# Kernel tuning notes

Hardware: AMD Instinct MI355X
Metric: run time of the kernel (lower is better)

The kernel has to match this reference:

```python
import jax, jax.numpy as jnp
import numpy as np

N_NODES = 50000
N_EDGES = 800000
IN_FEAT = 128
OUT_FEAT = 128


def _glorot(key, shape):
    fan_in, fan_out = shape[1], shape[0]
    lim = jnp.sqrt(6.0 / (fan_in + fan_out))
    return jax.random.uniform(key, shape, jnp.float32, -lim, lim)


def setup_inputs() -> dict:
    key = jax.random.key(0)
    ks = jax.random.split(key, 9)
    x = jax.random.normal(ks[0], (N_NODES, IN_FEAT), jnp.float32)
    edge_index = jax.random.randint(ks[1], (2, N_EDGES), 0, N_NODES, jnp.int64)
    # SAGEConv params: lin_l applied to aggregated neighbors (with bias),
    # lin_r applied to root features (no bias) -- PyG default mean aggregation.
    W1l = _glorot(ks[2], (OUT_FEAT, IN_FEAT)); b1l = jnp.zeros((OUT_FEAT,), jnp.float32)
    W1r = _glorot(ks[3], (OUT_FEAT, IN_FEAT))
    W2l = _glorot(ks[4], (OUT_FEAT, OUT_FEAT)); b2l = jnp.zeros((OUT_FEAT,), jnp.float32)
    W2r = _glorot(ks[5], (OUT_FEAT, OUT_FEAT))
    Wlin = _glorot(ks[6], (2, OUT_FEAT)); blin = jnp.zeros((2,), jnp.float32)
    return {"x": x, "edge_index": edge_index,
            "W1l": W1l, "b1l": b1l, "W1r": W1r,
            "W2l": W2l, "b2l": b2l, "W2r": W2r,
            "Wlin": Wlin, "blin": blin}


def _sage_conv(x, src, dst, Wl, bl, Wr, n_nodes):
    # mean-aggregate neighbor features at destination nodes
    agg_sum = jax.ops.segment_sum(x[src], dst, num_segments=n_nodes)  # [N, F]
    deg = jax.ops.segment_sum(jnp.ones((src.shape[0],), x.dtype), dst, num_segments=n_nodes)
    agg = agg_sum / jnp.maximum(deg, 1.0)[:, None]
    return agg @ Wl.T + bl + x @ Wr.T


def reference(x, edge_index, W1l, b1l, W1r, W2l, b2l, W2r, Wlin, blin):
    src, dst = edge_index[0], edge_index[1]
    n = x.shape[0]
    h = _sage_conv(x, src, dst, W1l, b1l, W1r, n)
    h = jax.nn.relu(h)  # dropout is identity in eval mode
    h = _sage_conv(h, src, dst, W2l, b2l, W2r, n)
    h = jax.nn.relu(h)
    logits = h @ Wlin.T + blin  # [N, 2]
    return jax.nn.log_softmax(logits, axis=1)
```

## Files before the change

kernel.cpp:

```cpp
#include <hip/hip_runtime.h>
#include <math.h>

#define N_NODES 50000
#define N_EDGES 800000
#define F 128
#define ELL_CAP 64
#define NSHARD 8
#define RANKS 128
#define EPR (N_EDGES / RANKS)
#define NPS (N_NODES / NSHARD)
#define EDGE_BLKS (NSHARD * RANKS)
#define CVT_BLKS 6250

typedef __attribute__((ext_vector_type(8))) short short8;
typedef __attribute__((ext_vector_type(4))) float float4v;

__device__ inline unsigned short f2bf(float f) {
    unsigned int u = __builtin_bit_cast(unsigned int, f);
    u += 0x7FFF + ((u >> 16) & 1);
    return (unsigned short)(u >> 16);
}
__device__ inline float bf2f_lo(unsigned int u) {
    return __builtin_bit_cast(float, u << 16);
}
__device__ inline float bf2f_hi(unsigned int u) {
    return __builtin_bit_cast(float, u & 0xFFFF0000u);
}

__global__ __launch_bounds__(256) void prep(const float* __restrict__ x,
                                            const int* __restrict__ src,
                                            const int* __restrict__ dst,
                                            const float* __restrict__ W1l,
                                            const float* __restrict__ W1r,
                                            const float* __restrict__ W2l,
                                            const float* __restrict__ W2r,
                                            unsigned short* __restrict__ xb,
                                            int* __restrict__ cnt,
                                            unsigned short* __restrict__ nbr,
                                            unsigned short* __restrict__ P1,
                                            unsigned short* __restrict__ P2) {
    int blk = blockIdx.x;
    if (blk < EDGE_BLKS) {
        int shard = blk & 7;
        int rank = blk >> 3;
        int lo = shard * NPS, hi = lo + NPS;
        int base = rank * EPR;
        for (int i = threadIdx.x; i < EPR; i += 256) {
            int d = dst[base + i];
            if (d >= lo && d < hi) {
                int s = src[base + i];
                int pos = atomicAdd(&cnt[d], 1);
                if (pos < ELL_CAP)
                    nbr[d * ELL_CAP + pos] = (unsigned short)s;
            }
        }
    } else if (blk < EDGE_BLKS + CVT_BLKS) {
        int i = (blk - EDGE_BLKS) * 256 + threadIdx.x;
        float4 v = ((const float4*)x)[i];
        unsigned int p0 = (unsigned int)f2bf(v.x) | ((unsigned int)f2bf(v.y) << 16);
        unsigned int p1 = (unsigned int)f2bf(v.z) | ((unsigned int)f2bf(v.w) << 16);
        ((uint2*)xb)[i] = make_uint2(p0, p1);
    } else {
        int pblk = blk - (EDGE_BLKS + CVT_BLKS);
        int t = (pblk & 15) * 256 + threadIdx.x;
        int lane = t & 63;
        int ct = (t >> 6) & 7;
        int ks = t >> 9;
        const float* Wl = (pblk < 16) ? W1l : W2l;
        const float* Wr = (pblk < 16) ? W1r : W2r;
        unsigned short* P = (pblk < 16) ? P1 : P2;
        int col = ct * 16 + (lane & 15);
        int kbase = (ks & 3) * 32 + (lane >> 4) * 8;
        const float* W = (ks < 4) ? Wl : Wr;
        unsigned short* dp = P + (size_t)t * 8;
        #pragma unroll
        for (int j = 0; j < 8; ++j) dp[j] = f2bf(W[col * F + kbase + j]);
    }
}

__global__ __launch_bounds__(256) void aggregate2(const unsigned short* __restrict__ X,
                                                  const int* __restrict__ cnt,
                                                  const unsigned short* __restrict__ nbr,
                                                  unsigned short* __restrict__ agg) {
    int tid = threadIdx.x;
    int wave = tid >> 6;
    int lane = tid & 63;
    int half = lane >> 5;
    int hl = lane & 31;
    int node = blockIdx.x * 8 + wave * 2 + half;

    int degt = cnt[node];
    int deg = degt < ELL_CAP ? degt : ELL_CAP;
    const unsigned short* nb = nbr + node * ELL_CAP;

    float a0 = 0.f, a1 = 0.f, a2 = 0.f, a3 = 0.f;
    int s = 0;
    for (; s + 4 <= deg; s += 4) {
        ushort4 nv = *(const ushort4*)(nb + s);
        uint2 g0 = *(const uint2*)(X + (size_t)nv.x * F + hl * 4);
        uint2 g1 = *(const uint2*)(X + (size_t)nv.y * F + hl * 4);
        uint2 g2 = *(const uint2*)(X + (size_t)nv.z * F + hl * 4);
        uint2 g3 = *(const uint2*)(X + (size_t)nv.w * F + hl * 4);
        a0 += bf2f_lo(g0.x) + bf2f_lo(g1.x) + bf2f_lo(g2.x) + bf2f_lo(g3.x);
        a1 += bf2f_hi(g0.x) + bf2f_hi(g1.x) + bf2f_hi(g2.x) + bf2f_hi(g3.x);
        a2 += bf2f_lo(g0.y) + bf2f_lo(g1.y) + bf2f_lo(g2.y) + bf2f_lo(g3.y);
        a3 += bf2f_hi(g0.y) + bf2f_hi(g1.y) + bf2f_hi(g2.y) + bf2f_hi(g3.y);
    }
    for (; s < deg; ++s) {
        int v = nb[s];
        uint2 g = *(const uint2*)(X + (size_t)v * F + hl * 4);
        a0 += bf2f_lo(g.x); a1 += bf2f_hi(g.x);
        a2 += bf2f_lo(g.y); a3 += bf2f_hi(g.y);
    }
    float inv = 1.0f / (float)(degt > 0 ? degt : 1);
    unsigned int p0 = (unsigned int)f2bf(a0 * inv) | ((unsigned int)f2bf(a1 * inv) << 16);
    unsigned int p1 = (unsigned int)f2bf(a2 * inv) | ((unsigned int)f2bf(a3 * inv) << 16);
    *(uint2*)(agg + (size_t)node * F + hl * 4) = make_uint2(p0, p1);
}

__global__ __launch_bounds__(256) void sage_gemm(const unsigned short* __restrict__ Abf,
                                                 const unsigned short* __restrict__ Bbf,
                                                 const unsigned short* __restrict__ Pw,
                                                 const float* __restrict__ bias,
                                                 unsigned short* __restrict__ Hout,
                                                 const float* __restrict__ Wlin,
                                                 const float* __restrict__ blin,
                                                 float* __restrict__ out, int mode) {
    int lane = threadIdx.x & 63;
    int wave = threadIdx.x >> 6;
    int r0 = blockIdx.x * 64 + wave * 16;
    int rowA = r0 + (lane & 15);
    if (rowA >= N_NODES) rowA = N_NODES - 1;
    int kg = lane >> 4;

    short8 af[4], bfr[4];
    const short8* Ap = (const short8*)(Abf + (size_t)rowA * F);
    const short8* Bp = (const short8*)(Bbf + (size_t)rowA * F);
    #pragma unroll
    for (int ks = 0; ks < 4; ++ks) {
        af[ks]  = Ap[ks * 4 + kg];
        bfr[ks] = Bp[ks * 4 + kg];
    }

    const short8* Wp = (const short8*)Pw;
    float4v acc[8];
    #pragma unroll
    for (int ct = 0; ct < 8; ++ct) {
        float4v c = {0.f, 0.f, 0.f, 0.f};
        #pragma unroll
        for (int ks = 0; ks < 4; ++ks)
            c = __builtin_amdgcn_mfma_f32_16x16x32_bf16(af[ks], Wp[(ks * 8 + ct) * 64 + lane], c, 0, 0, 0);
        #pragma unroll
        for (int ks = 0; ks < 4; ++ks)
            c = __builtin_amdgcn_mfma_f32_16x16x32_bf16(bfr[ks], Wp[((ks + 4) * 8 + ct) * 64 + lane], c, 0, 0, 0);
        acc[ct] = c;
    }

    int colb = lane & 15;
    int rq = lane >> 4;
    #pragma unroll
    for (int ct = 0; ct < 8; ++ct) {
        float bv = bias[ct * 16 + colb];
        #pragma unroll
        for (int i = 0; i < 4; ++i)
            acc[ct][i] = fmaxf(acc[ct][i] + bv, 0.f);
    }

    if (mode == 0) {
        #pragma unroll
        for (int ct = 0; ct < 8; ++ct) {
            #pragma unroll
            for (int i = 0; i < 4; ++i) {
                int row = r0 + rq * 4 + i;
                if (row < N_NODES)
                    Hout[(size_t)row * F + ct * 16 + colb] = f2bf(acc[ct][i]);
            }
        }
    } else {
        float w0[8], w1[8];
        #pragma unroll
        for (int ct = 0; ct < 8; ++ct) {
            w0[ct] = Wlin[ct * 16 + colb];
            w1[ct] = Wlin[F + ct * 16 + colb];
        }
        #pragma unroll
        for (int i = 0; i < 4; ++i) {
            float p0 = 0.f, p1 = 0.f;
            #pragma unroll
            for (int ct = 0; ct < 8; ++ct) {
                p0 += acc[ct][i] * w0[ct];
                p1 += acc[ct][i] * w1[ct];
            }
            #pragma unroll
            for (int off = 1; off < 16; off <<= 1) {
                p0 += __shfl_xor(p0, off);
                p1 += __shfl_xor(p1, off);
            }
            int row = r0 + rq * 4 + i;
            if (colb == 0 && row < N_NODES) {
                float a = p0 + blin[0];
                float b = p1 + blin[1];
                float m = fmaxf(a, b);
                float lse = m + logf(expf(a - m) + expf(b - m));
                out[(size_t)row * 2 + 0] = a - lse;
                out[(size_t)row * 2 + 1] = b - lse;
            }
        }
    }
}

extern "C" void kernel_launch(void* const* d_in, const int* in_sizes, int n_in,
                              void* d_out, int out_size, void* d_ws, size_t ws_size,
                              hipStream_t stream) {
    const float* x    = (const float*)d_in[0];
    const int*   ei   = (const int*)d_in[1];
    const float* W1l  = (const float*)d_in[2];
    const float* b1l  = (const float*)d_in[3];
    const float* W1r  = (const float*)d_in[4];
    const float* W2l  = (const float*)d_in[5];
    const float* b2l  = (const float*)d_in[6];
    const float* W2r  = (const float*)d_in[7];
    const float* Wlin = (const float*)d_in[8];
    const float* blin = (const float*)d_in[9];
    float* out = (float*)d_out;

    const int* src = ei;
    const int* dst = ei + N_EDGES;

    char* ws = (char*)d_ws;
    int*            cnt  = (int*)ws;
    unsigned short* nbr  = (unsigned short*)(ws + 262144);
    unsigned short* xb   = (unsigned short*)(ws + 6815744);
    unsigned short* h1b  = (unsigned short*)(ws + 19922944);
    unsigned short* aggb = (unsigned short*)(ws + 33030144);
    unsigned short* P1   = (unsigned short*)(ws + 46137344);
    unsigned short* P2   = (unsigned short*)(ws + 46202880);

    hipMemsetAsync(cnt, 0, N_NODES * sizeof(int), stream);

    prep<<<EDGE_BLKS + CVT_BLKS + 32, 256, 0, stream>>>(x, src, dst, W1l, W1r, W2l, W2r,
                                                        xb, cnt, nbr, P1, P2);

    aggregate2<<<6250, 256, 0, stream>>>(xb, cnt, nbr, aggb);
    sage_gemm<<<782, 256, 0, stream>>>(aggb, xb, P1, b1l, h1b, nullptr, nullptr, nullptr, 0);

    aggregate2<<<6250, 256, 0, stream>>>(h1b, cnt, nbr, aggb);
    sage_gemm<<<782, 256, 0, stream>>>(aggb, h1b, P2, b2l, nullptr, Wlin, blin, out, 1);
}
```

Measured before the change: 143.6 us.

## Build neighbor ELL via two-pass shared-memory bucketing instead of global atomics

```diff
diff --git a/kernel.cpp b/kernel.cpp
--- a/kernel.cpp
+++ b/kernel.cpp
@@ -9,6 +9,10 @@
 #define RANKS 128
 #define EPR (N_EDGES / RANKS)
 #define NPS (N_NODES / NSHARD)
+#define NBPS 25
+#define NBUCK (NSHARD * NBPS)
+#define BIN_CAP 80
+#define BUCK_CAP 4608
 #define EDGE_BLKS (NSHARD * RANKS)
 #define CVT_BLKS 6250
 
@@ -27,42 +31,64 @@
     return __builtin_bit_cast(float, u & 0xFFFF0000u);
 }
 
-__global__ __launch_bounds__(256) void prep(const float* __restrict__ x,
-                                            const int* __restrict__ src,
-                                            const int* __restrict__ dst,
-                                            const float* __restrict__ W1l,
-                                            const float* __restrict__ W1r,
-                                            const float* __restrict__ W2l,
-                                            const float* __restrict__ W2r,
-                                            unsigned short* __restrict__ xb,
-                                            int* __restrict__ cnt,
-                                            unsigned short* __restrict__ nbr,
-                                            unsigned short* __restrict__ P1,
-                                            unsigned short* __restrict__ P2) {
+__global__ __launch_bounds__(256) void prep1(const float* __restrict__ x,
+                                             const int* __restrict__ src,
+                                             const int* __restrict__ dst,
+                                             const float* __restrict__ W1l,
+                                             const float* __restrict__ W1r,
+                                             const float* __restrict__ W2l,
+                                             const float* __restrict__ W2r,
+                                             unsigned short* __restrict__ xb,
+                                             int* __restrict__ tails,
+                                             unsigned int* __restrict__ bucketEdges,
+                                             unsigned short* __restrict__ P1,
+                                             unsigned short* __restrict__ P2) {
     int blk = blockIdx.x;
+    int tid = threadIdx.x;
     if (blk < EDGE_BLKS) {
+        __shared__ int bin_cnt[NBPS];
+        __shared__ int bin_base[NBPS];
+        __shared__ unsigned int bins[NBPS * BIN_CAP];
         int shard = blk & 7;
         int rank = blk >> 3;
-        int lo = shard * NPS, hi = lo + NPS;
+        int lo = shard * NPS;
+        if (tid < NBPS) bin_cnt[tid] = 0;
+        __syncthreads();
         int base = rank * EPR;
-        for (int i = threadIdx.x; i < EPR; i += 256) {
+        for (int i = tid; i < EPR; i += 256) {
             int d = dst[base + i];
-            if (d >= lo && d < hi) {
+            unsigned int du = (unsigned int)(d - lo);
+            if (du < (unsigned int)NPS) {
                 int s = src[base + i];
-                int pos = atomicAdd(&cnt[d], 1);
-                if (pos < ELL_CAP)
-                    nbr[d * ELL_CAP + pos] = (unsigned short)s;
-            }
+                int lb = du >> 8;
+                int pos = atomicAdd(&bin_cnt[lb], 1);
+                if (pos < BIN_CAP)
+                    bins[lb * BIN_CAP + pos] = ((du & 255u) << 16) | (unsigned int)s;
+            }
+        }
+        __syncthreads();
+        if (tid < NBPS) {
+            int c = bin_cnt[tid]; if (c > BIN_CAP) c = BIN_CAP;
+            bin_cnt[tid] = c;
+            bin_base[tid] = atomicAdd(&tails[shard * NBPS + tid], c);
+        }
+        __syncthreads();
+        for (int b2 = 0; b2 < NBPS; ++b2) {
+            int c = bin_cnt[b2];
+            int rb = bin_base[b2];
+            unsigned int* dp = bucketEdges + (size_t)(shard * NBPS + b2) * BUCK_CAP;
+            for (int i = tid; i < c; i += 256)
+                if (rb + i < BUCK_CAP) dp[rb + i] = bins[b2 * BIN_CAP + i];
         }
     } else if (blk < EDGE_BLKS + CVT_BLKS) {
-        int i = (blk - EDGE_BLKS) * 256 + threadIdx.x;
+        int i = (blk - EDGE_BLKS) * 256 + tid;
         float4 v = ((const float4*)x)[i];
         unsigned int p0 = (unsigned int)f2bf(v.x) | ((unsigned int)f2bf(v.y) << 16);
         unsigned int p1 = (unsigned int)f2bf(v.z) | ((unsigned int)f2bf(v.w) << 16);
         ((uint2*)xb)[i] = make_uint2(p0, p1);
     } else {
         int pblk = blk - (EDGE_BLKS + CVT_BLKS);
-        int t = (pblk & 15) * 256 + threadIdx.x;
+        int t = (pblk & 15) * 256 + tid;
         int lane = t & 63;
         int ct = (t >> 6) & 7;
         int ks = t >> 9;
@@ -76,6 +102,35 @@
         #pragma unroll
         for (int j = 0; j < 8; ++j) dp[j] = f2bf(W[col * F + kbase + j]);
     }
+}
+
+__global__ __launch_bounds__(256) void ell_build(const int* __restrict__ tails,
+                                                 const unsigned int* __restrict__ bucketEdges,
+                                                 int* __restrict__ cnt,
+                                                 unsigned short* __restrict__ nbr) {
+    __shared__ int cl[256];
+    __shared__ unsigned short ell[256 * ELL_CAP];
+    int b = blockIdx.x;
+    int tid = threadIdx.x;
+    cl[tid] = 0;
+    __syncthreads();
+    int T = tails[b]; if (T > BUCK_CAP) T = BUCK_CAP;
+    const unsigned int* eb = bucketEdges + (size_t)b * BUCK_CAP;
+    for (int i = tid; i < T; i += 256) {
+        unsigned int rec = eb[i];
+        int nib = rec >> 16;
+        int pos = atomicAdd(&cl[nib], 1);
+        if (pos < ELL_CAP) ell[nib * ELL_CAP + pos] = (unsigned short)(rec & 0xFFFFu);
+    }
+    __syncthreads();
+    int shard = b / NBPS, lb = b % NBPS;
+    int nb0 = shard * NPS + lb * 256;
+    int nn = NPS - lb * 256; if (nn > 256) nn = 256;
+    if (tid < nn) cnt[nb0 + tid] = cl[tid];
+    const uint4* s4 = (const uint4*)ell;
+    uint4* d4 = (uint4*)(nbr + (size_t)nb0 * ELL_CAP);
+    int n4 = nn * (ELL_CAP * 2 / 16);
+    for (int i = tid; i < n4; i += 256) d4[i] = s4[i];
 }
 
 __global__ __launch_bounds__(256) void aggregate2(const unsigned short* __restrict__ X,
@@ -228,18 +283,21 @@
     const int* dst = ei + N_EDGES;
 
     char* ws = (char*)d_ws;
-    int*            cnt  = (int*)ws;
-    unsigned short* nbr  = (unsigned short*)(ws + 262144);
-    unsigned short* xb   = (unsigned short*)(ws + 6815744);
-    unsigned short* h1b  = (unsigned short*)(ws + 19922944);
-    unsigned short* aggb = (unsigned short*)(ws + 33030144);
-    unsigned short* P1   = (unsigned short*)(ws + 46137344);
-    unsigned short* P2   = (unsigned short*)(ws + 46202880);
-
-    hipMemsetAsync(cnt, 0, N_NODES * sizeof(int), stream);
-
-    prep<<<EDGE_BLKS + CVT_BLKS + 32, 256, 0, stream>>>(x, src, dst, W1l, W1r, W2l, W2r,
-                                                        xb, cnt, nbr, P1, P2);
+    int*            tails = (int*)ws;
+    unsigned int*   bEdge = (unsigned int*)(ws + 4096);
+    int*            cnt   = (int*)(ws + 3694592);
+    unsigned short* nbr   = (unsigned short*)(ws + 3895296);
+    unsigned short* xb    = (unsigned short*)(ws + 10296320);
+    unsigned short* h1b   = (unsigned short*)(ws + 23097344);
+    unsigned short* aggb  = (unsigned short*)(ws + 35898368);
+    unsigned short* P1    = (unsigned short*)(ws + 48699392);
+    unsigned short* P2    = (unsigned short*)(ws + 48764928);
+
+    hipMemsetAsync(tails, 0, NBUCK * sizeof(int), stream);
+
+    prep1<<<EDGE_BLKS + CVT_BLKS + 32, 256, 0, stream>>>(x, src, dst, W1l, W1r, W2l, W2r,
+                                                         xb, tails, bEdge, P1, P2);
+    ell_build<<<NBUCK, 256, 0, stream>>>(tails, bEdge, cnt, nbr);
 
     aggregate2<<<6250, 256, 0, stream>>>(xb, cnt, nbr, aggb);
     sage_gemm<<<782, 256, 0, stream>>>(aggb, xb, P1, b1l, h1b, nullptr, nullptr, nullptr, 0);
```

Result: faster. 137.9 us (-4.0%).
